# Optimization experiments

Hardware: AMD Instinct MI355X
Metric: run time of the kernel (lower is better)

Reference implementation:

```python
import jax, jax.numpy as jnp
import numpy as np

N, D, K = 65536, 64, 128   # points, feature dim, n_clusters
BETA = 0.0                 # distance weighting exponent offset
EPS = 1e-8


def pairwise_distance(a, b):
    # euclidean distance matrix [n, k]
    d2 = jnp.sum(a * a, 1)[:, None] + jnp.sum(b * b, 1)[None, :] - 2.0 * (a @ b.T)
    return jnp.sqrt(jnp.maximum(d2, 0.0))


def approx_cluster_filling(dist, beta):
    # differentiable soft cluster filling: inverse-distance weights with exponent (1+beta),
    # normalized per point, averaged over points -> [K]
    w = (dist + EPS) ** (-(1.0 + beta))
    w = w / jnp.sum(w, axis=1, keepdims=True)
    return jnp.mean(w, axis=0)


def wasserstein_distance(a, b):
    # sort-based per-feature 1D Wasserstein-1 distance, averaged over features
    return jnp.mean(jnp.abs(jnp.sort(a, axis=0) - jnp.sort(b, axis=0)))


def setup_inputs():
    key = jax.random.key(0)
    k1, k2, k3 = jax.random.split(key, 3)
    x = jax.random.normal(k1, (N, D), jnp.float32)
    target = jax.random.normal(k2, (N, D), jnp.float32)
    cluster_centers = jax.random.normal(k3, (K, D), jnp.float32)
    # precomputed target-side cluster statistics (LossKMeans.__init__, detached)
    dist_t = pairwise_distance(target, cluster_centers)
    prediction_target = jnp.argmin(dist_t, axis=1).astype(jnp.int32)
    filling_target = approx_cluster_filling(dist_t, BETA)
    return {"x": x, "target": target, "cluster_centers": cluster_centers,
            "prediction_target": prediction_target, "filling_target": filling_target}


def reference(x, target, cluster_centers, prediction_target, filling_target):
    # cluster-filling MSE (differentiable soft assignment)
    dist_x = pairwise_distance(x, cluster_centers)
    loss_fil = jnp.mean((approx_cluster_filling(dist_x, BETA) - filling_target) ** 2)
    # hard (detached) cluster assignment of x; concrete in eager mode
    pred_x = np.asarray(jnp.argmin(dist_x, axis=1))
    pred_t = np.asarray(prediction_target)
    loss_med = jnp.zeros((), jnp.float32)
    for c in np.unique(pred_x):  # data-dependent loop over occupied clusters (<= K)
        ix = np.nonzero(pred_x == c)[0]
        it = np.nonzero(pred_t == c)[0]
        m = min(ix.size, it.size)
        if m == 0:
            continue  # no matching target members -> skip (empty slices)
        loss_med = loss_med + wasserstein_distance(x[ix[:m]], target[it[:m]])
    return loss_fil + loss_med
```

## Files before the change

kernel.cpp:

```cpp
#include <hip/hip_runtime.h>
#include <math.h>

#define N_PTS 65536
#define DIM   64
#define K_CL  128
#define EPSV  1e-8f
#define CAP   8192


__global__ __launch_bounds__(256) void k_init(
    float* __restrict__ fill_acc, float* __restrict__ sumw,
    unsigned long long* __restrict__ pred_enc) {
  const int i = blockIdx.x * 256 + threadIdx.x;
  if (i < K_CL) fill_acc[i] = 0.0f;
  sumw[i] = 0.0f;
  pred_enc[i] = 0xFFFFFFFFFFFFFFFFull;
}

__global__ __launch_bounds__(256) void k_dist1(
    const float* __restrict__ x, const float* __restrict__ centers,
    float* __restrict__ sumw, unsigned long long* __restrict__ pred_enc,
    float* __restrict__ w)
{
  __shared__ float csq[32];
  const int kb    = blockIdx.x & 3;
  const int pb    = blockIdx.x >> 2;
  const int jbase = kb << 5;
  const int tid   = threadIdx.x;
  const int p     = pb * 256 + tid;

  if (tid < 32) {
    const float* cp = centers + (jbase + tid) * DIM;
    float s = 0.0f;
    #pragma unroll 8
    for (int d = 0; d < DIM; ++d) { float v = cp[d]; s += v * v; }
    csq[tid] = s;
  }

  float xr[DIM];
  const float4* xp = reinterpret_cast<const float4*>(x + (size_t)p * DIM);
  #pragma unroll
  for (int q = 0; q < DIM / 4; ++q) {
    float4 v = xp[q];
    xr[4 * q + 0] = v.x; xr[4 * q + 1] = v.y;
    xr[4 * q + 2] = v.z; xr[4 * q + 3] = v.w;
  }
  float xsq = 0.0f;
  #pragma unroll
  for (int d = 0; d < DIM; ++d) xsq += xr[d] * xr[d];
  __syncthreads();

  float sw = 0.0f, best = INFINITY;
  int   bj = jbase;
  #pragma unroll 2
  for (int jj = 0; jj < 32; ++jj) {
    const int j = jbase + jj;
    const float* cp = centers + j * DIM;
    float d0 = 0.f, d1 = 0.f, d2a = 0.f, d3 = 0.f;
    #pragma unroll
    for (int d = 0; d < DIM; d += 4) {
      d0  += xr[d + 0] * cp[d + 0];
      d1  += xr[d + 1] * cp[d + 1];
      d2a += xr[d + 2] * cp[d + 2];
      d3  += xr[d + 3] * cp[d + 3];
    }
    float dot  = (d0 + d1) + (d2a + d3);
    float dsq  = xsq + csq[jj] - 2.0f * dot;
    float dist = sqrtf(fmaxf(dsq, 0.0f));
    float ww   = 1.0f / (dist + EPSV);
    w[(size_t)j * N_PTS + p] = ww;
    sw += ww;
    if (dist < best) { best = dist; bj = j; }
  }
  atomicAdd(&sumw[p], sw);
  const unsigned long long enc =
      ((unsigned long long)__float_as_uint(best) << 32) | (unsigned int)bj;
  atomicMin(&pred_enc[p], enc);
}

__global__ __launch_bounds__(256) void k_pred(
    const unsigned long long* __restrict__ pred_enc,
    const float* __restrict__ sumw,
    int* __restrict__ pred_x, float* __restrict__ inv_sumw) {
  const int p = blockIdx.x * 256 + threadIdx.x;
  pred_x[p]   = (int)(pred_enc[p] & 0xFFFFFFFFull);
  inv_sumw[p] = 1.0f / sumw[p];
}

__global__ __launch_bounds__(256) void k_fill(
    const float* __restrict__ w, const float* __restrict__ inv_sumw,
    float* __restrict__ fill_acc)
{
  __shared__ float red[4];
  const int j    = blockIdx.x >> 3;
  const int seg  = blockIdx.x & 7;
  const int tid  = threadIdx.x;
  const float4* wj = reinterpret_cast<const float4*>(
      w + (size_t)j * N_PTS + seg * 8192);
  const float4* iv = reinterpret_cast<const float4*>(
      inv_sumw + seg * 8192);
  float s = 0.0f;
  #pragma unroll
  for (int q = 0; q < 8; ++q) {
    const int e = q * 256 + tid;
    float4 a = wj[e];
    float4 b = iv[e];
    s += a.x * b.x + a.y * b.y + a.z * b.z + a.w * b.w;
  }
  #pragma unroll
  for (int off = 32; off > 0; off >>= 1) s += __shfl_down(s, off);
  if ((tid & 63) == 0) red[tid >> 6] = s;
  __syncthreads();
  if (tid == 0)
    atomicAdd(&fill_acc[j], red[0] + red[1] + red[2] + red[3]);
}

__global__ __launch_bounds__(1024) void k_scatter(
    const int* __restrict__ pred_x, const int* __restrict__ pred_t,
    int* __restrict__ idx_x, int* __restrict__ idx_t,
    int* __restrict__ count_x, int* __restrict__ count_t)
{
  const int c    = blockIdx.x >> 1;
  const int side = blockIdx.x & 1;
  const int* __restrict__ pred = side ? pred_t : pred_x;
  int* __restrict__ out = side ? idx_t : idx_x;
  int* __restrict__ cnt = side ? count_t : count_x;

  __shared__ int wsum[16];
  const int tid = threadIdx.x, lane = tid & 63, w = tid >> 6;
  const int beg = w * 4096;

  int cw = 0;
  for (int s = 0; s < 4096; s += 64) {
    const bool m = (pred[beg + s + lane] == c);
    cw += __popcll(__ballot(m));
  }
  if (lane == 0) wsum[w] = cw;
  __syncthreads();
  int base = 0, tot = 0;
  #pragma unroll
  for (int k = 0; k < 16; ++k) { int v = wsum[k]; tot += v; if (k < w) base += v; }

  int run = base;
  for (int s = 0; s < 4096; s += 64) {
    const int i = beg + s + lane;
    const bool m = (pred[i] == c);
    unsigned long long bal = __ballot(m);
    int lp = __popcll(bal & ((1ull << lane) - 1ull));
    if (m) { int pos = run + lp; if (pos < CAP) out[c * CAP + pos] = i; }
    run += __popcll(bal);
  }
  if (tid == 0) cnt[c] = tot;
}

__global__ __launch_bounds__(128) void k_offsets(
    const int* __restrict__ count_x, const int* __restrict__ count_t,
    int* __restrict__ offc)
{
  __shared__ int sm[128];
  const int tid = threadIdx.x;
  const int m  = min(min(count_x[tid], CAP), min(count_t[tid], CAP));
  const int sz = ((m + 3) & ~3) * DIM;
  sm[tid] = sz;
  __syncthreads();
  for (int s = 1; s < 128; s <<= 1) {
    int v = (tid >= s) ? sm[tid - s] : 0;
    __syncthreads();
    sm[tid] += v;
    __syncthreads();
  }
  offc[tid] = sm[tid] - sz;
}

__global__ __launch_bounds__(256) void k_gather_t(
    const float* __restrict__ x, const float* __restrict__ t,
    const int* __restrict__ idx_x, const int* __restrict__ idx_t,
    const int* __restrict__ count_x, const int* __restrict__ count_t,
    const int* __restrict__ offc,
    float* __restrict__ gxT, float* __restrict__ gtT)
{
  const int wid  = blockIdx.x * 4 + (threadIdx.x >> 6);
  const int lane = threadIdx.x & 63;
  const int side = wid >> 14;
  const int c    = (wid >> 7) & 127;
  const int q    = wid & 127;
  const int m = min(min(count_x[c], CAP), min(count_t[c], CAP));
  if (q * 64 >= m) return;
  const int r  = q * 64 + lane;
  const int mp = (m + 3) & ~3;
  const float* __restrict__ src = side ? t : x;
  const int*   __restrict__ idx = side ? idx_t : idx_x;
  float* __restrict__ dst = (side ? gtT : gxT) + offc[c];
  if (r < m) {
    const float4* rp =
        reinterpret_cast<const float4*>(src + (size_t)idx[c * CAP + r] * DIM);
    float v[DIM];
    #pragma unroll
    for (int qq = 0; qq < DIM / 4; ++qq) {
      float4 f = rp[qq];
      v[4*qq+0]=f.x; v[4*qq+1]=f.y; v[4*qq+2]=f.z; v[4*qq+3]=f.w;
    }
    #pragma unroll
    for (int d = 0; d < DIM; ++d) dst[(size_t)d * mp + r] = v[d];
  }
}

__device__ __forceinline__ void ce(float& a, float& b, bool up) {
  float lo = fminf(a, b), hi = fmaxf(a, b);
  a = up ? lo : hi;
  b = up ? hi : lo;
}

__device__ __forceinline__ void merge8(float* v, bool up) {
  ce(v[0],v[4],up); ce(v[1],v[5],up); ce(v[2],v[6],up); ce(v[3],v[7],up);
  ce(v[0],v[2],up); ce(v[1],v[3],up); ce(v[4],v[6],up); ce(v[5],v[7],up);
  ce(v[0],v[1],up); ce(v[2],v[3],up); ce(v[4],v[5],up); ce(v[6],v[7],up);
}

__device__ __forceinline__ void sort8(float* v, bool up8) {
  ce(v[0],v[1],true );  ce(v[2],v[3],false); ce(v[4],v[5],true );  ce(v[6],v[7],false);
  ce(v[0],v[2],true );  ce(v[1],v[3],true );  ce(v[4],v[6],false); ce(v[5],v[7],false);
  ce(v[0],v[1],true );  ce(v[2],v[3],true );  ce(v[4],v[5],false); ce(v[6],v[7],false);
  merge8(v, up8);
}

__device__ __forceinline__ void merge16(float* v, bool up) {
  #pragma unroll
  for (int e = 0; e < 8; ++e) ce(v[e], v[e + 8], up);
  merge8(v, up);
  merge8(v + 8, up);
}

__device__ __forceinline__ void sort16(float* v, bool up16) {
  sort8(v, true);
  sort8(v + 8, false);
  merge16(v, up16);
}

__device__ __forceinline__ void stage_pair8(float va[8], float vb[8],
                                            int ib, int k, bool up) {
  #pragma unroll
  for (int j = (k >> 1) > 256 ? 256 : (k >> 1); j >= 8; j >>= 1) {
    const int  jl = j >> 3;
    const bool tm = (up == ((ib & j) == 0));
    #pragma unroll
    for (int e = 0; e < 8; ++e) {
      float p = __shfl_xor(va[e], jl, 64);
      va[e] = tm ? fminf(va[e], p) : fmaxf(va[e], p);
      float q = __shfl_xor(vb[e], jl, 64);
      vb[e] = tm ? fminf(vb[e], q) : fmaxf(vb[e], q);
    }
  }
  merge8(va, up);
  merge8(vb, up);
}

__device__ __forceinline__ void stage_pair16(float va[16], float vb[16],
                                             int ib, int k, bool up) {
  #pragma unroll
  for (int j = (k >> 1) > 512 ? 512 : (k >> 1); j >= 16; j >>= 1) {
    const int  jl = j >> 4;
    const bool tm = (up == ((ib & j) == 0));
    #pragma unroll
    for (int e = 0; e < 16; ++e) {
      float p = __shfl_xor(va[e], jl, 64);
      va[e] = tm ? fminf(va[e], p) : fmaxf(va[e], p);
      float q = __shfl_xor(vb[e], jl, 64);
      vb[e] = tm ? fminf(vb[e], q) : fmaxf(vb[e], q);
    }
  }
  merge16(va, up);
  merge16(vb, up);
}

__device__ __forceinline__ void stage_one16(float v[16], int ib, int k, bool up) {
  #pragma unroll
  for (int j = (k >> 1) > 512 ? 512 : (k >> 1); j >= 16; j >>= 1) {
    const int  jl = j >> 4;
    const bool tm = (up == ((ib & j) == 0));
    #pragma unroll
    for (int e = 0; e < 16; ++e) {
      float p = __shfl_xor(v[e], jl, 64);
      v[e] = tm ? fminf(v[e], p) : fmaxf(v[e], p);
    }
  }
  merge16(v, up);
}

__device__ __forceinline__ void load8c(const float* __restrict__ col,
                                       int ib, int m, float v[8]) {
  if (ib + 7 < m) {
    #pragma unroll
    for (int q = 0; q < 2; ++q) {
      float4 f = *(const float4*)&col[ib + 4 * q];
      v[4*q+0]=f.x; v[4*q+1]=f.y; v[4*q+2]=f.z; v[4*q+3]=f.w;
    }
  } else {
    #pragma unroll
    for (int e = 0; e < 8; ++e) v[e] = (ib + e < m) ? col[ib + e] : INFINITY;
  }
}

__device__ __forceinline__ void load16c(const float* __restrict__ col,
                                        int ib, int m, float v[16]) {
  if (ib + 15 < m) {
    #pragma unroll
    for (int q = 0; q < 4; ++q) {
      float4 f = *(const float4*)&col[ib + 4 * q];
      v[4*q+0]=f.x; v[4*q+1]=f.y; v[4*q+2]=f.z; v[4*q+3]=f.w;
    }
  } else {
    #pragma unroll
    for (int e = 0; e < 16; ++e) v[e] = (ib + e < m) ? col[ib + e] : INFINITY;
  }
}

template<int P>
__device__ __forceinline__ void sort_col(float v[16], int ib, bool act,
                                         const float* __restrict__ col,
                                         int m, float* __restrict__ sa) {
  if (act) {
    load16c(col, ib, m, v);
    sort16(v, ((ib & 16) == 0));
    #pragma unroll
    for (int k = 32; k <= 1024; k <<= 1)
      stage_one16(v, ib, k, ((ib & k) == 0));
  }
  #pragma unroll
  for (int k = 2048; k <= P; k <<= 1) {
    const bool up = ((ib & k) == 0);
    #pragma unroll
    for (int j = k >> 1; j >= 1024; j >>= 1) {
      __syncthreads();
      if (act) {
        #pragma unroll
        for (int q = 0; q < 4; ++q)
          *(float4*)&sa[ib + 4*q] =
              make_float4(v[4*q], v[4*q+1], v[4*q+2], v[4*q+3]);
      }
      __syncthreads();
      if (act) {
        const int pi = ib ^ j;
        const bool tm = (up == ((ib & j) == 0));
        #pragma unroll
        for (int q = 0; q < 4; ++q) {
          float4 A = *(const float4*)&sa[pi + 4*q];
          v[4*q+0] = tm ? fminf(v[4*q+0],A.x) : fmaxf(v[4*q+0],A.x);
          v[4*q+1] = tm ? fminf(v[4*q+1],A.y) : fmaxf(v[4*q+1],A.y);
          v[4*q+2] = tm ? fminf(v[4*q+2],A.z) : fmaxf(v[4*q+2],A.z);
          v[4*q+3] = tm ? fminf(v[4*q+3],A.w) : fmaxf(v[4*q+3],A.w);
        }
      }
    }
    if (act) stage_one16(v, ib, k, up);
  }
}

template<int P>
__device__ __forceinline__ float task_body(const float* colx, const float* colt,
                                           int m, int tid, float* sa) {
  const int ib = tid << 4;
  const bool act = (ib < P);
  float va[16], vb[16];
  sort_col<P>(va, ib, act, colx, m, sa);
  sort_col<P>(vb, ib, act, colt, m, sa);
  float s = 0.0f;
  if (act) {
    #pragma unroll
    for (int e = 0; e < 16; ++e)
      if (ib + e < m) s += fabsf(va[e] - vb[e]);
  }
  return s;
}

__global__ __launch_bounds__(512) void k_w1(
    const float* __restrict__ gxT, const float* __restrict__ gtT,
    const int* __restrict__ offc,
    const int* __restrict__ count_x, const int* __restrict__ count_t,
    float* __restrict__ parts)
{
  __shared__ float sa[8192];
  __shared__ float red[8];
  const int tid = threadIdx.x;

  if (blockIdx.x < 8192) {
    const int task = blockIdx.x;
    const int c = task >> 6, d = task & 63;
    const int m = min(min(count_x[c], CAP), min(count_t[c], CAP));
    if (m <= 1024) return;
    const int mp = (m + 3) & ~3;
    const float* colx = gxT + offc[c] + (size_t)d * mp;
    const float* colt = gtT + offc[c] + (size_t)d * mp;

    float s;
    if (m <= 2048)      s = task_body<2048>(colx, colt, m, tid, sa);
    else if (m <= 4096) s = task_body<4096>(colx, colt, m, tid, sa);
    else                s = task_body<8192>(colx, colt, m, tid, sa);

    #pragma unroll
    for (int off = 32; off > 0; off >>= 1) s += __shfl_down(s, off);
    __syncthreads();
    if ((tid & 63) == 0) red[tid >> 6] = s;
    __syncthreads();
    if (tid == 0) {
      float tot = 0.0f;
      #pragma unroll
      for (int w = 0; w < 8; ++w) tot += red[w];
      parts[task] = tot / (float)(m * DIM);
    }
  } else {
    const int task = (blockIdx.x - 8192) * 8 + (tid >> 6);
    const int lane = tid & 63;
    const int c = task >> 6, d = task & 63;
    const int m = min(min(count_x[c], CAP), min(count_t[c], CAP));
    if (m > 1024) return;
    if (m == 0) { if (lane == 0) parts[task] = 0.0f; return; }
    const int mp = (m + 3) & ~3;
    const float* colx = gxT + offc[c] + (size_t)d * mp;
    const float* colt = gtT + offc[c] + (size_t)d * mp;

    float s = 0.0f;
    if (m <= 512) {
      const int ib = lane << 3;
      float va[8], vb[8];
      load8c(colx, ib, m, va);
      load8c(colt, ib, m, vb);
      const bool u8 = ((ib & 8) == 0);
      sort8(va, u8);
      sort8(vb, u8);
      #pragma unroll
      for (int k = 16; k <= 512; k <<= 1)
        stage_pair8(va, vb, ib, k, ((ib & k) == 0));
      #pragma unroll
      for (int e = 0; e < 8; ++e)
        if (ib + e < m) s += fabsf(va[e] - vb[e]);
    } else {
      const int ib = lane << 4;
      float va[16], vb[16];
      load16c(colx, ib, m, va);
      load16c(colt, ib, m, vb);
      const bool u16 = ((ib & 16) == 0);
      sort16(va, u16);
      sort16(vb, u16);
      #pragma unroll
      for (int k = 32; k <= 1024; k <<= 1)
        stage_pair16(va, vb, ib, k, ((ib & k) == 0));
      #pragma unroll
      for (int e = 0; e < 16; ++e)
        if (ib + e < m) s += fabsf(va[e] - vb[e]);
    }
    #pragma unroll
    for (int off = 32; off > 0; off >>= 1) s += __shfl_down(s, off);
    if (lane == 0) parts[task] = s / (float)(m * DIM);
  }
}

__global__ __launch_bounds__(1024) void k_final(
    const float* __restrict__ fill_acc, const float* __restrict__ ft,
    const float* __restrict__ parts, float* __restrict__ out)
{
  __shared__ float red[16];
  const int tid = threadIdx.x;
  float s = 0.0f;
  #pragma unroll
  for (int i = 0; i < 8; ++i) s += parts[tid + i * 1024];
  if (tid < K_CL) {
    float v = fill_acc[tid] * (1.0f / (float)N_PTS) - ft[tid];
    s += v * v * (1.0f / (float)K_CL);
  }
  #pragma unroll
  for (int off = 32; off > 0; off >>= 1) s += __shfl_down(s, off);
  if ((tid & 63) == 0) red[tid >> 6] = s;
  __syncthreads();
  if (tid == 0) {
    float tot = 0.0f;
    #pragma unroll
    for (int w = 0; w < 16; ++w) tot += red[w];
    out[0] = tot;
  }
}

extern "C" void kernel_launch(void* const* d_in, const int* in_sizes, int n_in,
                              void* d_out, int out_size, void* d_ws, size_t ws_size,
                              hipStream_t stream)
{
  (void)in_sizes; (void)n_in; (void)out_size; (void)ws_size;
  const float* x      = (const float*)d_in[0];
  const float* target = (const float*)d_in[1];
  const float* cc     = (const float*)d_in[2];
  const int*   pred_t = (const int*)d_in[3];
  const float* ft     = (const float*)d_in[4];
  float* out = (float*)d_out;

  char* ws = (char*)d_ws;
  float* fill_acc = (float*)(ws + 0);
  int*   pred_x   = (int*)(ws + 1024);
  int*   idx_x    = (int*)(ws + 263168);
  int*   idx_t    = (int*)(ws + 4457472);
  int*   count_x  = (int*)(ws + 8651776);
  int*   count_t  = (int*)(ws + 8651776 + 512);
  float* parts    = (float*)(ws + 8652800);
  float* sumw     = (float*)(ws + 8685568);
  float* inv_sumw = (float*)(ws + 8947712);
  unsigned long long* pred_enc = (unsigned long long*)(ws + 9209856);
  int*   offc     = (int*)(ws + 9732096);
  float* gxT      = (float*)(ws + 9732608);
  float* gtT      = (float*)(ws + 26640896);
  float* wmat     = (float*)(ws + 9732608);

  k_init<<<N_PTS / 256, 256, 0, stream>>>(fill_acc, sumw, pred_enc);
  k_dist1<<<N_PTS / 256 * 4, 256, 0, stream>>>(x, cc, sumw, pred_enc, wmat);
  k_pred<<<N_PTS / 256, 256, 0, stream>>>(pred_enc, sumw, pred_x, inv_sumw);
  k_fill<<<K_CL * 8, 256, 0, stream>>>(wmat, inv_sumw, fill_acc);
  k_scatter<<<K_CL * 2, 1024, 0, stream>>>(pred_x, pred_t, idx_x, idx_t,
                                           count_x, count_t);
  k_offsets<<<1, 128, 0, stream>>>(count_x, count_t, offc);
  k_gather_t<<<8192, 256, 0, stream>>>(x, target, idx_x, idx_t,
                                       count_x, count_t, offc, gxT, gtT);
  k_w1<<<8192 + 1024, 512, 0, stream>>>(gxT, gtT, offc,
                                        count_x, count_t, parts);
  k_final<<<1, 1024, 0, stream>>>(fill_acc, ft, parts, out);
}
```

Baseline: 342.4 us.

## Split W1 kernel into independent per-side column sort and separate diff-reduce kernel

The fused sort-and-compare kernel is replaced by two kernels. k_sort sorts each x and target column independently and in place, which doubles the number of blocks and wavefronts and halves the register footprint per sort. k_diff then reads both sorted columns and reduces the absolute differences. Small columns now sort only up to the next power of two instead of a fixed 512 width. The cost is an extra global write and read of the gathered data plus one more kernel launch.

After: 323.6 us. 1.06x faster.

```diff
diff --git a/kernel.cpp b/kernel.cpp
--- a/kernel.cpp
+++ b/kernel.cpp
@@ -97,8 +97,7 @@
   const int tid  = threadIdx.x;
   const float4* wj = reinterpret_cast<const float4*>(
       w + (size_t)j * N_PTS + seg * 8192);
-  const float4* iv = reinterpret_cast<const float4*>(
-      inv_sumw + seg * 8192);
+  const float4* iv = reinterpret_cast<const float4*>(inv_sumw + seg * 8192);
   float s = 0.0f;
   #pragma unroll
   for (int q = 0; q < 8; ++q) {
@@ -237,40 +236,17 @@
   merge16(v, up16);
 }
 
-__device__ __forceinline__ void stage_pair8(float va[8], float vb[8],
-                                            int ib, int k, bool up) {
-  #pragma unroll
+__device__ __forceinline__ void stage_one8(float v[8], int ib, int k, bool up) {
   for (int j = (k >> 1) > 256 ? 256 : (k >> 1); j >= 8; j >>= 1) {
     const int  jl = j >> 3;
     const bool tm = (up == ((ib & j) == 0));
     #pragma unroll
     for (int e = 0; e < 8; ++e) {
-      float p = __shfl_xor(va[e], jl, 64);
-      va[e] = tm ? fminf(va[e], p) : fmaxf(va[e], p);
-      float q = __shfl_xor(vb[e], jl, 64);
-      vb[e] = tm ? fminf(vb[e], q) : fmaxf(vb[e], q);
-    }
-  }
-  merge8(va, up);
-  merge8(vb, up);
-}
-
-__device__ __forceinline__ void stage_pair16(float va[16], float vb[16],
-                                             int ib, int k, bool up) {
-  #pragma unroll
-  for (int j = (k >> 1) > 512 ? 512 : (k >> 1); j >= 16; j >>= 1) {
-    const int  jl = j >> 4;
-    const bool tm = (up == ((ib & j) == 0));
-    #pragma unroll
-    for (int e = 0; e < 16; ++e) {
-      float p = __shfl_xor(va[e], jl, 64);
-      va[e] = tm ? fminf(va[e], p) : fmaxf(va[e], p);
-      float q = __shfl_xor(vb[e], jl, 64);
-      vb[e] = tm ? fminf(vb[e], q) : fmaxf(vb[e], q);
-    }
-  }
-  merge16(va, up);
-  merge16(vb, up);
+      float p = __shfl_xor(v[e], jl, 64);
+      v[e] = tm ? fminf(v[e], p) : fmaxf(v[e], p);
+    }
+  }
+  merge8(v, up);
 }
 
 __device__ __forceinline__ void stage_one16(float v[16], int ib, int k, bool up) {
@@ -357,102 +333,117 @@
 }
 
 template<int P>
-__device__ __forceinline__ float task_body(const float* colx, const float* colt,
-                                           int m, int tid, float* sa) {
+__device__ __forceinline__ void sort_col_io(float* __restrict__ col,
+                                            int m, int mp, int tid,
+                                            float* __restrict__ sa) {
   const int ib = tid << 4;
   const bool act = (ib < P);
-  float va[16], vb[16];
-  sort_col<P>(va, ib, act, colx, m, sa);
-  sort_col<P>(vb, ib, act, colt, m, sa);
-  float s = 0.0f;
+  float v[16];
+  sort_col<P>(v, ib, act, col, m, sa);
   if (act) {
     #pragma unroll
-    for (int e = 0; e < 16; ++e)
-      if (ib + e < m) s += fabsf(va[e] - vb[e]);
-  }
-  return s;
-}
-
-__global__ __launch_bounds__(512) void k_w1(
+    for (int q = 0; q < 4; ++q)
+      if (ib + 4 * q < mp)
+        *(float4*)&col[ib + 4*q] =
+            make_float4(v[4*q], v[4*q+1], v[4*q+2], v[4*q+3]);
+  }
+}
+
+__global__ __launch_bounds__(512) void k_sort(
+    float* __restrict__ gxT, float* __restrict__ gtT,
+    const int* __restrict__ offc,
+    const int* __restrict__ count_x, const int* __restrict__ count_t)
+{
+  __shared__ float sa[8192];
+  const int tid = threadIdx.x;
+
+  if (blockIdx.x < 16384) {
+    const int side = blockIdx.x >> 13;
+    const int cd   = blockIdx.x & 8191;
+    const int c = cd >> 6, d = cd & 63;
+    const int m = min(min(count_x[c], CAP), min(count_t[c], CAP));
+    if (m <= 1024) return;
+    const int mp = (m + 3) & ~3;
+    float* col = (side ? gtT : gxT) + offc[c] + (size_t)d * mp;
+    if (m <= 2048)      sort_col_io<2048>(col, m, mp, tid, sa);
+    else if (m <= 4096) sort_col_io<4096>(col, m, mp, tid, sa);
+    else                sort_col_io<8192>(col, m, mp, tid, sa);
+  } else {
+    const int base = (blockIdx.x - 16384) * 8 + (tid >> 6);
+    const int lane = tid & 63;
+    const int side = base >> 13;
+    const int cd   = base & 8191;
+    const int c = cd >> 6, d = cd & 63;
+    const int m = min(min(count_x[c], CAP), min(count_t[c], CAP));
+    if (m > 1024 || m == 0) return;
+    const int mp = (m + 3) & ~3;
+    float* col = (side ? gtT : gxT) + offc[c] + (size_t)d * mp;
+
+    if (m <= 512) {
+      int P = 8;
+      while (P < m) P <<= 1;
+      const int ib = lane << 3;
+      float v[8];
+      load8c(col, ib, m, v);
+      sort8(v, ((ib & 8) == 0));
+      for (int k = 16; k <= P; k <<= 1)
+        stage_one8(v, ib, k, ((ib & k) == 0));
+      #pragma unroll
+      for (int q = 0; q < 2; ++q)
+        if (ib + 4 * q < mp)
+          *(float4*)&col[ib + 4*q] =
+              make_float4(v[4*q], v[4*q+1], v[4*q+2], v[4*q+3]);
+    } else {
+      const int ib = lane << 4;
+      float v[16];
+      load16c(col, ib, m, v);
+      sort16(v, ((ib & 16) == 0));
+      #pragma unroll
+      for (int k = 32; k <= 1024; k <<= 1)
+        stage_one16(v, ib, k, ((ib & k) == 0));
+      #pragma unroll
+      for (int q = 0; q < 4; ++q)
+        if (ib + 4 * q < mp)
+          *(float4*)&col[ib + 4*q] =
+              make_float4(v[4*q], v[4*q+1], v[4*q+2], v[4*q+3]);
+    }
+  }
+}
+
+__global__ __launch_bounds__(256) void k_diff(
     const float* __restrict__ gxT, const float* __restrict__ gtT,
     const int* __restrict__ offc,
     const int* __restrict__ count_x, const int* __restrict__ count_t,
     float* __restrict__ parts)
 {
-  __shared__ float sa[8192];
-  __shared__ float red[8];
+  __shared__ float red[4];
+  const int task = blockIdx.x;
+  const int c = task >> 6, d = task & 63;
+  const int m = min(min(count_x[c], CAP), min(count_t[c], CAP));
   const int tid = threadIdx.x;
-
-  if (blockIdx.x < 8192) {
-    const int task = blockIdx.x;
-    const int c = task >> 6, d = task & 63;
-    const int m = min(min(count_x[c], CAP), min(count_t[c], CAP));
-    if (m <= 1024) return;
-    const int mp = (m + 3) & ~3;
-    const float* colx = gxT + offc[c] + (size_t)d * mp;
-    const float* colt = gtT + offc[c] + (size_t)d * mp;
-
-    float s;
-    if (m <= 2048)      s = task_body<2048>(colx, colt, m, tid, sa);
-    else if (m <= 4096) s = task_body<4096>(colx, colt, m, tid, sa);
-    else                s = task_body<8192>(colx, colt, m, tid, sa);
-
-    #pragma unroll
-    for (int off = 32; off > 0; off >>= 1) s += __shfl_down(s, off);
-    __syncthreads();
-    if ((tid & 63) == 0) red[tid >> 6] = s;
-    __syncthreads();
-    if (tid == 0) {
-      float tot = 0.0f;
-      #pragma unroll
-      for (int w = 0; w < 8; ++w) tot += red[w];
-      parts[task] = tot / (float)(m * DIM);
-    }
-  } else {
-    const int task = (blockIdx.x - 8192) * 8 + (tid >> 6);
-    const int lane = tid & 63;
-    const int c = task >> 6, d = task & 63;
-    const int m = min(min(count_x[c], CAP), min(count_t[c], CAP));
-    if (m > 1024) return;
-    if (m == 0) { if (lane == 0) parts[task] = 0.0f; return; }
-    const int mp = (m + 3) & ~3;
-    const float* colx = gxT + offc[c] + (size_t)d * mp;
-    const float* colt = gtT + offc[c] + (size_t)d * mp;
-
-    float s = 0.0f;
-    if (m <= 512) {
-      const int ib = lane << 3;
-      float va[8], vb[8];
-      load8c(colx, ib, m, va);
-      load8c(colt, ib, m, vb);
-      const bool u8 = ((ib & 8) == 0);
-      sort8(va, u8);
-      sort8(vb, u8);
-      #pragma unroll
-      for (int k = 16; k <= 512; k <<= 1)
-        stage_pair8(va, vb, ib, k, ((ib & k) == 0));
-      #pragma unroll
-      for (int e = 0; e < 8; ++e)
-        if (ib + e < m) s += fabsf(va[e] - vb[e]);
+  if (m == 0) { if (tid == 0) parts[task] = 0.0f; return; }
+  const int mp = (m + 3) & ~3;
+  const float* colx = gxT + offc[c] + (size_t)d * mp;
+  const float* colt = gtT + offc[c] + (size_t)d * mp;
+  float s = 0.0f;
+  for (int r = tid * 4; r < mp; r += 1024) {
+    float4 a = *(const float4*)&colx[r];
+    float4 b = *(const float4*)&colt[r];
+    if (r + 3 < m) {
+      s += fabsf(a.x-b.x) + fabsf(a.y-b.y) + fabsf(a.z-b.z) + fabsf(a.w-b.w);
     } else {
-      const int ib = lane << 4;
-      float va[16], vb[16];
-      load16c(colx, ib, m, va);
-      load16c(colt, ib, m, vb);
-      const bool u16 = ((ib & 16) == 0);
-      sort16(va, u16);
-      sort16(vb, u16);
-      #pragma unroll
-      for (int k = 32; k <= 1024; k <<= 1)
-        stage_pair16(va, vb, ib, k, ((ib & k) == 0));
-      #pragma unroll
-      for (int e = 0; e < 16; ++e)
-        if (ib + e < m) s += fabsf(va[e] - vb[e]);
-    }
-    #pragma unroll
-    for (int off = 32; off > 0; off >>= 1) s += __shfl_down(s, off);
-    if (lane == 0) parts[task] = s / (float)(m * DIM);
-  }
+      if (r + 0 < m) s += fabsf(a.x - b.x);
+      if (r + 1 < m) s += fabsf(a.y - b.y);
+      if (r + 2 < m) s += fabsf(a.z - b.z);
+      if (r + 3 < m) s += fabsf(a.w - b.w);
+    }
+  }
+  #pragma unroll
+  for (int off = 32; off > 0; off >>= 1) s += __shfl_down(s, off);
+  if ((tid & 63) == 0) red[tid >> 6] = s;
+  __syncthreads();
+  if (tid == 0)
+    parts[task] = (red[0] + red[1] + red[2] + red[3]) / (float)(m * DIM);
 }
 
 __global__ __launch_bounds__(1024) void k_final(
@@ -503,10 +494,10 @@
   float* sumw     = (float*)(ws + 8685568);
   float* inv_sumw = (float*)(ws + 8947712);
   unsigned long long* pred_enc = (unsigned long long*)(ws + 9209856);
-  int*   offc     = (int*)(ws + 9732096);
-  float* gxT      = (float*)(ws + 9732608);
-  float* gtT      = (float*)(ws + 26640896);
-  float* wmat     = (float*)(ws + 9732608);
+  int*   offc     = (int*)(ws + 9734144);
+  float* gxT      = (float*)(ws + 9735168);
+  float* gtT      = (float*)(ws + 26643456);
+  float* wmat     = (float*)(ws + 9735168);
 
   k_init<<<N_PTS / 256, 256, 0, stream>>>(fill_acc, sumw, pred_enc);
   k_dist1<<<N_PTS / 256 * 4, 256, 0, stream>>>(x, cc, sumw, pred_enc, wmat);
@@ -517,7 +508,8 @@
   k_offsets<<<1, 128, 0, stream>>>(count_x, count_t, offc);
   k_gather_t<<<8192, 256, 0, stream>>>(x, target, idx_x, idx_t,
                                        count_x, count_t, offc, gxT, gtT);
-  k_w1<<<8192 + 1024, 512, 0, stream>>>(gxT, gtT, offc,
-                                        count_x, count_t, parts);
+  k_sort<<<16384 + 2048, 512, 0, stream>>>(gxT, gtT, offc, count_x, count_t);
+  k_diff<<<K_CL * DIM, 256, 0, stream>>>(gxT, gtT, offc,
+                                         count_x, count_t, parts);
   k_final<<<1, 1024, 0, stream>>>(fill_acc, ft, parts, out);
 }
```
